# Performance work log

Hardware: AMD Instinct MI355X
Metric: run time of the kernel (lower is better)

Reference implementation:

```python
import jax, jax.numpy as jnp
import numpy as np

EMBED_DIM = 1024
NUM_HEADS = 16
HEAD_DIM = EMBED_DIM // NUM_HEADS
B, T = 4, 2048


def setup_inputs() -> dict:
    key = jax.random.key(0)
    ks = jax.random.split(key, 5)
    s = 1.0 / np.sqrt(EMBED_DIM)
    x = jax.random.normal(ks[0], (B, T, EMBED_DIM), dtype=jnp.float32)
    attention_mask = jnp.ones((B, 1, 1, T), dtype=jnp.int32)
    # torch Linear weights: qkv (3E, E), out (E, E); store transposed for x @ W
    W_qkv = jax.random.uniform(ks[1], (EMBED_DIM, 3 * EMBED_DIM), jnp.float32, -s, s)
    b_qkv = jax.random.uniform(ks[2], (3 * EMBED_DIM,), jnp.float32, -s, s)
    W_out = jax.random.uniform(ks[3], (EMBED_DIM, EMBED_DIM), jnp.float32, -s, s)
    b_out = jax.random.uniform(ks[4], (EMBED_DIM,), jnp.float32, -s, s)
    return {"x": x, "attention_mask": attention_mask,
            "W_qkv": W_qkv, "b_qkv": b_qkv, "W_out": W_out, "b_out": b_out}


def reference(x, attention_mask, W_qkv, b_qkv, W_out, b_out):
    Bq, Tq, E = x.shape
    qkv = x @ W_qkv + b_qkv                              # [B,T,3E]
    qkv = qkv.reshape(Bq, Tq, 3, NUM_HEADS, HEAD_DIM)
    qkv = jnp.transpose(qkv, (2, 0, 3, 1, 4))            # [3,B,H,T,d]
    q, k, v = qkv[0], qkv[1], qkv[2]
    scores = jnp.einsum('bhqd,bhkd->bhqk', q, k) / jnp.sqrt(
        jnp.asarray(HEAD_DIM, x.dtype))                  # [B,H,T,T]
    scores = jnp.where(attention_mask == 0, jnp.asarray(-jnp.inf, x.dtype), scores)
    attn = jax.nn.softmax(scores, axis=-1)
    ctx = jnp.einsum('bhqk,bhkd->bhqd', attn, v)         # [B,H,T,d]
    ctx = jnp.transpose(ctx, (0, 2, 1, 3)).reshape(Bq, Tq, E)
    return ctx @ W_out + b_out
```

## Files before the change

kernel.cpp:

```cpp
#include <hip/hip_runtime.h>
#include <hip/hip_bf16.h>
#include <stdint.h>


typedef __attribute__((ext_vector_type(8))) short short8;
typedef __attribute__((ext_vector_type(4))) float f32x4;
typedef __attribute__((ext_vector_type(16))) float f32x16;
typedef __attribute__((ext_vector_type(4))) unsigned short ushort4_t;
typedef __attribute__((ext_vector_type(8))) unsigned short ushort8_t;

#define SEQ 2048
#define EDIM 1024
#define QSCALE 0.18033688011112042f

__device__ __forceinline__ unsigned short f2bf(float x) {
  union { float f; uint32_t u; } v; v.f = x;
  uint32_t r = v.u + 0x7fffu + ((v.u >> 16) & 1u);
  return (unsigned short)(r >> 16);
}

__device__ __forceinline__ uint32_t cvtpk(float lo, float hi) {
  uint32_t r;
  asm("v_cvt_pk_bf16_f32 %0, %1, %2" : "=v"(r) : "v"(lo), "v"(hi));
  return r;
}

__device__ __forceinline__ float exp2_raw(float x) {
  float r;
  asm("v_exp_f32 %0, %1" : "=v"(r) : "v"(x));
  return r;
}

__device__ __forceinline__ void gload_lds16(const void* g, void* l) {
  typedef __attribute__((address_space(1))) const unsigned int gu32;
  typedef __attribute__((address_space(3))) unsigned int lu32;
  __builtin_amdgcn_global_load_lds((gu32*)g, (lu32*)l, 16, 0, 0);
}

__global__ void k_prep(const float* __restrict__ x,
                       unsigned short* __restrict__ xb,
                       const float* __restrict__ Wq,
                       unsigned short* __restrict__ wqt,
                       const float* __restrict__ Wo,
                       unsigned short* __restrict__ wot) {
  __shared__ float tile[32][33];
  const int id = blockIdx.x;
  if (id < 4096) {
    const int i = id * 256 + threadIdx.x;
    const float4* p = ((const float4*)x) + (size_t)i * 2;
    float4 a = p[0], b = p[1];
    ushort8_t v;
    v[0] = f2bf(a.x); v[1] = f2bf(a.y); v[2] = f2bf(a.z); v[3] = f2bf(a.w);
    v[4] = f2bf(b.x); v[5] = f2bf(b.y); v[6] = f2bf(b.z); v[7] = f2bf(b.w);
    ((ushort8_t*)xb)[i] = v;
    return;
  }
  const float* W;
  unsigned short* Wt;
  int N, bx, by;
  if (id < 7168) { W = Wq; Wt = wqt; N = 3072; bx = (id - 4096) % 96; by = (id - 4096) / 96; }
  else           { W = Wo; Wt = wot; N = 1024; bx = (id - 7168) % 32; by = (id - 7168) / 32; }
  const int K = 1024;
  const int c0 = bx * 32, r0 = by * 32;
  const int tx = threadIdx.x & 31, ty = threadIdx.x >> 5;
#pragma unroll
  for (int i = 0; i < 4; ++i) {
    int r = ty + i * 8;
    tile[r][tx] = W[(size_t)(r0 + r) * N + c0 + tx];
  }
  __syncthreads();
#pragma unroll
  for (int i = 0; i < 4; ++i) {
    int r = ty + i * 8;
    Wt[(size_t)(c0 + r) * K + r0 + tx] = f2bf(tile[tx][r]);
  }
}

template <int EPI, int NBX>
__global__ __launch_bounds__(256, 2) void k_gemm(
    const unsigned short* __restrict__ A, const unsigned short* __restrict__ Bt,
    const float* __restrict__ bias, unsigned short* __restrict__ Qo,
    unsigned short* __restrict__ Ko, unsigned short* __restrict__ VTo,
    float* __restrict__ Out) {
  __shared__ unsigned short As[2][2][128 * 32];
  __shared__ unsigned short Bs[2][2][128 * 32];
  const int tid = threadIdx.x;
  const int lane = tid & 63, wid = tid >> 6;
  const int wr = wid >> 1, wc = wid & 1;
  const int g = lane >> 4, r = lane & 15;
  const int lid = blockIdx.y * NBX + blockIdx.x;
  const int total = NBX * gridDim.y;
  const int id = (lid & 7) * (total >> 3) + (lid >> 3);
  const int m0 = (id / NBX) * 128, n0 = (id % NBX) * 128;

  const int row0 = tid >> 2, sl0 = tid & 3;
  const unsigned short* a0 = A + (size_t)(m0 + row0) * 1024 + sl0 * 8;
  const unsigned short* a1 = A + (size_t)(m0 + 64 + row0) * 1024 + sl0 * 8;
  const unsigned short* b0 = Bt + (size_t)(n0 + row0) * 1024 + sl0 * 8;
  const unsigned short* b1 = Bt + (size_t)(n0 + 64 + row0) * 1024 + sl0 * 8;
  char* adst = (char*)As + wid * 64 * 16;
  char* bdst = (char*)Bs + wid * 64 * 16;

  auto STAGE = [&](int buf) {
    const int bo = buf * 16384;
    gload_lds16(a0,      adst + bo);
    gload_lds16(a1,      adst + bo + 4096);
    gload_lds16(a0 + 32, adst + bo + 8192);
    gload_lds16(a1 + 32, adst + bo + 8192 + 4096);
    gload_lds16(b0,      bdst + bo);
    gload_lds16(b1,      bdst + bo + 4096);
    gload_lds16(b0 + 32, bdst + bo + 8192);
    gload_lds16(b1 + 32, bdst + bo + 8192 + 4096);
    a0 += 64; a1 += 64; b0 += 64; b1 += 64;
  };

  f32x4 zero4 = {0.f, 0.f, 0.f, 0.f};
  f32x4 acc[4][4];
#pragma unroll
  for (int mi = 0; mi < 4; ++mi)
#pragma unroll
    for (int ni = 0; ni < 4; ++ni) acc[mi][ni] = zero4;

  STAGE(0);
  asm volatile("s_waitcnt vmcnt(0)" ::: "memory");
  __builtin_amdgcn_s_barrier();

  for (int t = 0; t < 16; ++t) {
    const int cur = t & 1;
    if (t < 15) STAGE(cur ^ 1);
#pragma unroll
    for (int sub = 0; sub < 2; ++sub) {
      short8 af[4], bf[4];
#pragma unroll
      for (int mi = 0; mi < 4; ++mi)
        af[mi] = *(const short8*)&As[cur][sub][(wr * 64 + mi * 16 + r) * 32 + g * 8];
#pragma unroll
      for (int ni = 0; ni < 4; ++ni)
        bf[ni] = *(const short8*)&Bs[cur][sub][(wc * 64 + ni * 16 + r) * 32 + g * 8];
#pragma unroll
      for (int mi = 0; mi < 4; ++mi)
#pragma unroll
        for (int ni = 0; ni < 4; ++ni)
          acc[mi][ni] = __builtin_amdgcn_mfma_f32_16x16x32_bf16(
              af[mi], bf[ni], acc[mi][ni], 0, 0, 0);
    }
    asm volatile("s_waitcnt vmcnt(0)" ::: "memory");
    __builtin_amdgcn_s_barrier();
  }

#pragma unroll
  for (int mi = 0; mi < 4; ++mi) {
#pragma unroll
    for (int ni = 0; ni < 4; ++ni) {
      const int n = n0 + wc * 64 + ni * 16 + r;
      const float bv = bias[n];
      const int mbase = m0 + wr * 64 + mi * 16 + g * 4;
      if (EPI == 0) {
        const int sec = n >> 10, e = n & 1023, h = e >> 6, dd = e & 63;
        const int b = mbase >> 11, t = mbase & 2047;
        if (sec == 2) {
          ushort4_t pk;
#pragma unroll
          for (int j = 0; j < 4; ++j) pk[j] = f2bf(acc[mi][ni][j] + bv);
          *(ushort4_t*)&VTo[(((size_t)b * 16 + h) * 64 + dd) * 2048 + t] = pk;
        } else {
          unsigned short* dst = (sec == 0) ? Qo : Ko;
          const float scl = (sec == 0) ? QSCALE : 1.0f;
#pragma unroll
          for (int j = 0; j < 4; ++j)
            dst[(((size_t)b * 16 + h) * 2048 + t + j) * 64 + dd] =
                f2bf((acc[mi][ni][j] + bv) * scl);
        }
      } else {
#pragma unroll
        for (int j = 0; j < 4; ++j)
          Out[(size_t)(mbase + j) * 1024 + n] = acc[mi][ni][j] + bv;
      }
    }
  }
}

__global__ __launch_bounds__(512, 4) void k_attn(
    const unsigned short* __restrict__ Qg, const unsigned short* __restrict__ Kg,
    const unsigned short* __restrict__ VTg, const int* __restrict__ maskp,
    unsigned short* __restrict__ ctx) {
  __shared__ unsigned short Ks[2 * 4096];
  __shared__ unsigned short Vs[2 * 4096];
  const int tid = threadIdx.x, lane = tid & 63, wid = tid >> 6;
  const int q = lane & 31, hi = lane >> 5;
  const int id = blockIdx.x;
  const int slot = id >> 3;
  const int bh = (id & 7) * 8 + (slot >> 3);
  const int b = bh >> 4, h = bh & 15;
  const int q0 = (slot & 7) * 256 + wid * 32;
  const int qr = q0 + q;

  const unsigned short* Qb = Qg + (size_t)bh * SEQ * 64;
  const unsigned short* Kb = Kg + (size_t)bh * SEQ * 64;
  const unsigned short* Vb = VTg + (size_t)bh * 64 * SEQ;
  const int* mb = maskp + b * SEQ;

  const int srow = tid >> 3, sc = tid & 7;
  const unsigned short* kp = Kb + srow * 64 + sc * 8;
  const unsigned short* vp = Vb + (size_t)srow * SEQ + sc * 8;
  const int pslot = ((sc >> 1) * 128 + (srow >> 5) * 64 + (sc & 1) * 32 +
                     (srow & 31)) ^ (sc & 7);
  char* kw = (char*)Ks + pslot * 16;
  char* vw = (char*)Vs + pslot * 16;

  short8 qf[4];
#pragma unroll
  for (int ds = 0; ds < 4; ++ds)
    qf[ds] = *(const short8*)&Qb[(size_t)qr * 64 + ds * 16 + hi * 8];

  short8 onesf;
#pragma unroll
  for (int j = 0; j < 8; ++j) onesf[j] = (short)0x3F80;

  f32x16 z16 = {0.f,0.f,0.f,0.f,0.f,0.f,0.f,0.f,0.f,0.f,0.f,0.f,0.f,0.f,0.f,0.f};
  f32x16 o0 = z16, o1 = z16;
  f32x16 osum = z16;
  const int kb4 = hi * 4;

  {
    short8 kreg = *(const short8*)kp;  kp += 4096;
    short8 vreg = *(const short8*)vp;  vp += 64;
    *(short8*)kw = kreg;
    *(short8*)vw = vreg;
  }
  const int* mptr = mb + lane;
  int mv = mptr[0];
  mptr += 64;
  __syncthreads();

  for (int t = 0; t < 32; ++t) {
    const int cur = t & 1;
    short8 kreg = *(const short8*)kp;
    short8 vreg = *(const short8*)vp;
    const int mvn = mptr[0];
    if (t < 30) { kp += 4096; vp += 64; mptr += 64; }
    const unsigned long long bits = __ballot(mv != 0);
    mv = mvn;

    const char* KsB = (const char*)Ks + cur * 8192;
    const char* VsB = (const char*)Vs + cur * 8192;
    f32x16 c0 = z16, c1 = z16;
    __builtin_amdgcn_s_setprio(1);
#pragma unroll
    for (int ds = 0; ds < 4; ++ds) {
      const int ko = (lane ^ ((ds * 2 + hi) & 7)) * 16 + ds * 2048;
      short8 ka0 = *(const short8*)(KsB + ko);
      short8 ka1 = *(const short8*)(KsB + ko + 1024);
      c0 = __builtin_amdgcn_mfma_f32_32x32x16_bf16(ka0, qf[ds], c0, 0, 0, 0);
      c1 = __builtin_amdgcn_mfma_f32_32x32x16_bf16(ka1, qf[ds], c1, 0, 0, 0);
    }
    __builtin_amdgcn_s_setprio(0);

    {
      const int bo = (cur ^ 1) * 8192;
      *(short8*)(kw + bo) = kreg;
      *(short8*)(vw + bo) = vreg;
    }

#pragma unroll
    for (int i = 0; i < 16; ++i) {
      c0[i] = exp2_raw(c0[i]);
      c1[i] = exp2_raw(c1[i]);
    }
    if (bits != ~0ull) {
#pragma unroll
      for (int i = 0; i < 16; ++i) {
        const int k0 = (i & 3) + 8 * (i >> 2) + kb4;
        if (!((bits >> k0) & 1)) c0[i] = 0.f;
        if (!((bits >> (k0 + 32)) & 1)) c1[i] = 0.f;
      }
    }

    short8 pf[4];
#pragma unroll
    for (int sub = 0; sub < 2; ++sub) {
      uint32_t w[8];
#pragma unroll
      for (int j = 0; j < 8; ++j)
        w[j] = sub ? cvtpk(c1[2 * j], c1[2 * j + 1])
                   : cvtpk(c0[2 * j], c0[2 * j + 1]);
      asm("v_permlane32_swap_b32 %0, %1" : "+v"(w[0]), "+v"(w[2]));
      asm("v_permlane32_swap_b32 %0, %1" : "+v"(w[1]), "+v"(w[3]));
      asm("v_permlane32_swap_b32 %0, %1" : "+v"(w[4]), "+v"(w[6]));
      asm("v_permlane32_swap_b32 %0, %1" : "+v"(w[5]), "+v"(w[7]));
      union { uint32_t u[4]; short8 s; } ua, ub;
      ua.u[0] = w[0]; ua.u[1] = w[1]; ua.u[2] = w[2]; ua.u[3] = w[3];
      ub.u[0] = w[4]; ub.u[1] = w[5]; ub.u[2] = w[6]; ub.u[3] = w[7];
      pf[sub * 2] = ua.s;
      pf[sub * 2 + 1] = ub.s;
    }

    __builtin_amdgcn_s_setprio(1);
#pragma unroll
    for (int ks = 0; ks < 4; ++ks) {
      const int vo = (lane ^ ((ks * 2 + hi) & 7)) * 16 + ks * 2048;
      short8 va0 = *(const short8*)(VsB + vo);
      short8 va1 = *(const short8*)(VsB + vo + 1024);
      o0 = __builtin_amdgcn_mfma_f32_32x32x16_bf16(va0, pf[ks], o0, 0, 0, 0);
      o1 = __builtin_amdgcn_mfma_f32_32x32x16_bf16(va1, pf[ks], o1, 0, 0, 0);
      osum = __builtin_amdgcn_mfma_f32_32x32x16_bf16(onesf, pf[ks], osum,
                                                     0, 0, 0);
    }
    __builtin_amdgcn_s_setprio(0);

    __syncthreads();
  }

  const float inv = 1.f / osum[0];
#pragma unroll
  for (int ns = 0; ns < 2; ++ns) {
#pragma unroll
    for (int g_ = 0; g_ < 4; ++g_) {
      ushort4_t v4;
#pragma unroll
      for (int e = 0; e < 4; ++e) {
        const float val = (ns ? o1[g_ * 4 + e] : o0[g_ * 4 + e]) * inv;
        v4[e] = f2bf(val);
      }
      *(ushort4_t*)&ctx[((size_t)b * SEQ + qr) * 1024 + h * 64 + ns * 32 +
                        g_ * 8 + hi * 4] = v4;
    }
  }
}

extern "C" void kernel_launch(void* const* d_in, const int* in_sizes, int n_in,
                              void* d_out, int out_size, void* d_ws,
                              size_t ws_size, hipStream_t stream) {
  const float* x = (const float*)d_in[0];
  const int* mask = (const int*)d_in[1];
  const float* Wqkv = (const float*)d_in[2];
  const float* bqkv = (const float*)d_in[3];
  const float* Wout = (const float*)d_in[4];
  const float* bout = (const float*)d_in[5];
  float* out = (float*)d_out;

  unsigned short* ws = (unsigned short*)d_ws;
  unsigned short* xb = ws;
  unsigned short* wqt = ws + 8388608;
  unsigned short* wot = ws + 11534336;
  unsigned short* Q = ws + 12582912;
  unsigned short* K = ws + 20971520;
  unsigned short* VT = ws + 29360128;
  unsigned short* ctx = xb;

  k_prep<<<8192, 256, 0, stream>>>(x, xb, Wqkv, wqt, Wout, wot);
  k_gemm<0, 24><<<dim3(24, 64), 256, 0, stream>>>(xb, wqt, bqkv, Q, K, VT,
                                                  nullptr);
  k_attn<<<512, 512, 0, stream>>>(Q, K, VT, mask, ctx);
  k_gemm<1, 8><<<dim3(8, 64), 256, 0, stream>>>(ctx, wot, bout, nullptr,
                                                nullptr, nullptr, out);
}
```

Measured before the change: 188.9 us.

## Process two K/V tiles per barrier in attention kernel with larger LDS stages

The attention loop now loads and computes two 64-key tiles per iteration, with double-buffered LDS stages twice as large, so it runs 16 iterations with one __syncthreads each instead of 32. The aim is to halve the barrier count and give more slack to hide global loads. In exchange, LDS use per block doubles and launch bounds drop from 4 to 2 blocks per CU, which lowers occupancy and may raise register pressure.

New measurement: 184.3 us. -2.5%, faster.

```diff
diff --git a/kernel.cpp b/kernel.cpp
--- a/kernel.cpp
+++ b/kernel.cpp
@@ -180,12 +180,12 @@
   }
 }
 
-__global__ __launch_bounds__(512, 4) void k_attn(
+__global__ __launch_bounds__(512, 2) void k_attn(
     const unsigned short* __restrict__ Qg, const unsigned short* __restrict__ Kg,
     const unsigned short* __restrict__ VTg, const int* __restrict__ maskp,
     unsigned short* __restrict__ ctx) {
-  __shared__ unsigned short Ks[2 * 4096];
-  __shared__ unsigned short Vs[2 * 4096];
+  __shared__ unsigned short Ks[2 * 8192];
+  __shared__ unsigned short Vs[2 * 8192];
   const int tid = threadIdx.x, lane = tid & 63, wid = tid >> 6;
   const int q = lane & 31, hi = lane >> 5;
   const int id = blockIdx.x;
@@ -222,28 +222,8 @@
   f32x16 osum = z16;
   const int kb4 = hi * 4;
 
-  {
-    short8 kreg = *(const short8*)kp;  kp += 4096;
-    short8 vreg = *(const short8*)vp;  vp += 64;
-    *(short8*)kw = kreg;
-    *(short8*)vw = vreg;
-  }
-  const int* mptr = mb + lane;
-  int mv = mptr[0];
-  mptr += 64;
-  __syncthreads();
-
-  for (int t = 0; t < 32; ++t) {
-    const int cur = t & 1;
-    short8 kreg = *(const short8*)kp;
-    short8 vreg = *(const short8*)vp;
-    const int mvn = mptr[0];
-    if (t < 30) { kp += 4096; vp += 64; mptr += 64; }
-    const unsigned long long bits = __ballot(mv != 0);
-    mv = mvn;
-
-    const char* KsB = (const char*)Ks + cur * 8192;
-    const char* VsB = (const char*)Vs + cur * 8192;
+  auto COMPUTE = [&](const char* KsB, const char* VsB,
+                     unsigned long long bits) {
     f32x16 c0 = z16, c1 = z16;
     __builtin_amdgcn_s_setprio(1);
 #pragma unroll
@@ -255,12 +235,6 @@
       c1 = __builtin_amdgcn_mfma_f32_32x32x16_bf16(ka1, qf[ds], c1, 0, 0, 0);
     }
     __builtin_amdgcn_s_setprio(0);
-
-    {
-      const int bo = (cur ^ 1) * 8192;
-      *(short8*)(kw + bo) = kreg;
-      *(short8*)(vw + bo) = vreg;
-    }
 
 #pragma unroll
     for (int i = 0; i < 16; ++i) {
@@ -307,6 +281,46 @@
                                                      0, 0, 0);
     }
     __builtin_amdgcn_s_setprio(0);
+  };
+
+  {
+    short8 kA = *(const short8*)kp;
+    short8 kB = *(const short8*)(kp + 4096);
+    short8 vA = *(const short8*)vp;
+    short8 vB = *(const short8*)(vp + 64);
+    kp += 8192; vp += 128;
+    *(short8*)kw = kA;            *(short8*)(kw + 8192) = kB;
+    *(short8*)vw = vA;            *(short8*)(vw + 8192) = vB;
+  }
+  const int* mptr = mb + lane;
+  int mv0 = mptr[0], mv1 = mptr[64];
+  mptr += 128;
+  __syncthreads();
+
+  for (int t = 0; t < 16; ++t) {
+    const int cur = t & 1;
+    short8 kA = *(const short8*)kp;
+    short8 kB = *(const short8*)(kp + 4096);
+    short8 vA = *(const short8*)vp;
+    short8 vB = *(const short8*)(vp + 64);
+    const int mn0 = mptr[0], mn1 = mptr[64];
+    if (t < 14) { kp += 8192; vp += 128; mptr += 128; }
+    const unsigned long long bits0 = __ballot(mv0 != 0);
+    const unsigned long long bits1 = __ballot(mv1 != 0);
+    mv0 = mn0; mv1 = mn1;
+
+    const char* KsC = (const char*)Ks + cur * 16384;
+    const char* VsC = (const char*)Vs + cur * 16384;
+
+    COMPUTE(KsC, VsC, bits0);
+
+    {
+      const int bo = (cur ^ 1) * 16384;
+      *(short8*)(kw + bo) = kA;          *(short8*)(kw + bo + 8192) = kB;
+      *(short8*)(vw + bo) = vA;          *(short8*)(vw + bo + 8192) = vB;
+    }
+
+    COMPUTE(KsC + 8192, VsC + 8192, bits1);
 
     __syncthreads();
   }
```
